# Kernel optimization log

Hardware: AMD Instinct MI355X
Metric: run time of the kernel (lower is better)

## Reference

```python
import jax, jax.numpy as jnp
import numpy as np

RAY_DIR = jnp.array([0.4395064455, 0.617598629942, 0.652231566745], dtype=jnp.float32)
TOL = 1e-7
CONTACT_THRESH = 25.0   # opt.contact_thresh
COLLISION_THRESH = 25.0  # opt.collision_thresh
BIG = 1e10


def mesh_contains(points, triangles, tri_valid):
    """Moller-Trumbore ray casting (fixed ray dir), parity test.
    points [B,P,3], triangles [B,T,3,3], tri_valid [B,T] -> exterior [B,P] bool."""
    v0, v1, v2 = triangles[:, :, 0, :], triangles[:, :, 1, :], triangles[:, :, 2, :]
    e1 = v1 - v0
    e2 = v2 - v0
    pvec = jnp.cross(jnp.broadcast_to(RAY_DIR, e2.shape), e2)          # [B,T,3]
    dets = jnp.sum(e1 * pvec, -1)                                      # [B,T]
    parallel = jnp.abs(dets) < TOL
    invdet = 1.0 / (dets + 0.1 * TOL)
    tvec = points[:, None, :, :] - v0[:, :, None, :]                   # [B,T,P,3]
    u = jnp.sum(tvec * pvec[:, :, None, :], -1) * invdet[:, :, None]   # [B,T,P]
    qvec = jnp.cross(tvec, e1[:, :, None, :])                          # [B,T,P,3]
    v = jnp.sum(qvec * RAY_DIR, -1) * invdet[:, :, None]
    t = jnp.sum(e2[:, :, None, :] * qvec, -1) * invdet[:, :, None]
    inter = (u > 0) & (u < 1) & (v > 0) & (u + v < 1) & (t > TOL)
    inter = inter & (~parallel & tri_valid)[:, :, None]
    n_hits = jnp.sum(inter.astype(jnp.int32), axis=1)                  # [B,P]
    return (n_hits % 2) == 0


def masked_mean_loss(vals, mask):
    m = mask.astype(vals.dtype)
    tot = m.sum()
    loss = jnp.where(tot > 0, (m * vals).sum() / jnp.maximum(tot, 1.0), 0.0)
    row = m.sum(1)
    losses = jnp.where(row > 0, (m * vals).sum(1) / jnp.maximum(row, 1.0), 0.0)
    return loss, losses


def setup_inputs() -> dict:
    key = jax.random.key(0)
    ks = jax.random.split(key, 6)
    B, Nh, Fh, No, Fo = 8, 778, 1538, 2000, 4000
    hand_verts = jax.random.normal(ks[0], (B, Nh, 3), dtype=jnp.float32)
    hand_faces = jax.random.randint(ks[1], (B, Fh, 3), 0, Nh, dtype=jnp.int32)
    obj_verts = jax.random.normal(ks[2], (B, No, 3), dtype=jnp.float32)
    obj_faces = jax.random.randint(ks[3], (B, Fo, 3), 0, 1200, dtype=jnp.int32)
    obj_vert_splits = 1200 + jax.random.randint(ks[4], (B,), 0, No - 1200 + 1, dtype=jnp.int32)
    obj_face_splits = 2400 + jax.random.randint(ks[5], (B,), 0, Fo - 2400 + 1, dtype=jnp.int32)
    return {"hand_verts": hand_verts, "hand_faces": hand_faces,
            "obj_verts": obj_verts, "obj_faces": obj_faces,
            "obj_vert_splits": obj_vert_splits, "obj_face_splits": obj_face_splits}


def reference(hand_verts, hand_faces, obj_verts, obj_faces, obj_vert_splits, obj_face_splits):
    B, Nh, _ = hand_verts.shape
    No = obj_verts.shape[1]
    Fo = obj_faces.shape[1]
    sg = jax.lax.stop_gradient

    # gather triangles (batched)
    hand_tri = jax.vmap(lambda v, f: v[f])(hand_verts, hand_faces)     # [B,Fh,3,3]
    obj_tri = jax.vmap(lambda v, f: v[f])(obj_verts, obj_faces)        # [B,Fo,3,3]

    face_valid = jnp.arange(Fo)[None, :] < obj_face_splits[:, None]    # [B,Fo]
    vert_valid = jnp.arange(No)[None, :] < obj_vert_splits[:, None]    # [B,No]

    # containment tests run on detached geometry (as in original)
    hand_tri_valid = jnp.ones(hand_tri.shape[:2], dtype=bool)
    exterior_obj = mesh_contains(sg(obj_verts), sg(hand_tri), hand_tri_valid)   # [B,No]
    exterior_hand = mesh_contains(sg(hand_verts), sg(obj_tri), face_valid)      # [B,Nh]

    penetr_o_mask = (~exterior_obj) & vert_valid
    penetr_h_mask = ~exterior_hand

    # ragged squared pairwise distances (bmm form of original), padded cols -> BIG
    rx = jnp.sum(hand_verts * hand_verts, -1)                          # [B,Nh]
    ry = jnp.sum(obj_verts * obj_verts, -1)                            # [B,No]
    zz = jnp.einsum('bnd,bmd->bnm', hand_verts, obj_verts)             # [B,Nh,No]
    dists = rx[:, :, None] + ry[:, None, :] - 2.0 * zz
    dists = jnp.where(vert_valid[:, None, :], dists, BIG)

    minoh_idxs = jnp.argmin(dists, axis=1)                             # [B,No]
    minho_idxs = jnp.argmin(dists, axis=2)                             # [B,Nh]

    results_close = jnp.take_along_axis(obj_verts, minho_idxs[:, :, None], axis=1)    # [B,Nh,3]
    results_o_close = jnp.take_along_axis(hand_verts, minoh_idxs[:, :, None], axis=1)  # [B,No,3]

    # contact_target == 'all'
    anchor_dists = jnp.sqrt(jnp.sum((results_close - hand_verts) ** 2, -1))    # [B,Nh]
    anchor_o_dist = jnp.sqrt(jnp.sum((results_o_close - obj_verts) ** 2, -1))  # [B,No]

    # contact_mode == 'dist_tanh' -> below_dist all ones
    contact_vals = CONTACT_THRESH * jnp.tanh(anchor_dists / CONTACT_THRESH)
    # collision_mode == 'dist_tanh'
    collision_vals = COLLISION_THRESH * jnp.tanh(anchor_dists / COLLISION_THRESH)
    collision_o_vals = COLLISION_THRESH * jnp.tanh(anchor_o_dist / COLLISION_THRESH)
    collision_o_vals = jnp.where(vert_valid, collision_o_vals, 0.0)

    # contact_zones == 'all'
    missed_mask = exterior_hand

    missed_loss, missed_losses = masked_mean_loss(contact_vals, missed_mask)
    penetr_h_loss, penetr_h_losses = masked_mean_loss(collision_vals, penetr_h_mask)
    penetr_o_loss, penetr_o_losses = masked_mean_loss(collision_o_vals, penetr_o_mask)
    penetr_loss = penetr_h_loss + penetr_o_loss
    penetr_losses = penetr_h_losses + penetr_o_losses

    return missed_loss, penetr_loss, missed_losses, penetr_losses
```

## Files before the change

### kernel.cpp

```cpp
#include <hip/hip_runtime.h>
#include <hip/hip_bf16.h>


#define RX 0.4395064455f
#define RY 0.617598629942f
#define RZ 0.652231566745f

#define MAXCHUNK_F4 512

struct Params {
    const float* hand_verts; const int* hand_faces;
    const float* obj_verts;  const int* obj_faces;
    const int* ovsplit; const int* ofsplit;
    int* hitsA;
    int* hitsB;
    float* anchor_h; float* anchor_o; float* partials;
    float* out;
    int B, Nh, Fh, No, Fo;
    int pbA, CA, chunkA, blocksA;
    int pbB, CB, chunkB, blocksB;
};

__device__ __forceinline__ void tri_pre_one(const float* __restrict__ vb,
                                            const int* __restrict__ f,
                                            float4* o) {
#pragma clang fp contract(off)
    int i0 = f[0], i1 = f[1], i2 = f[2];
    float v0x = vb[i0*3+0], v0y = vb[i0*3+1], v0z = vb[i0*3+2];
    float v1x = vb[i1*3+0], v1y = vb[i1*3+1], v1z = vb[i1*3+2];
    float v2x = vb[i2*3+0], v2y = vb[i2*3+1], v2z = vb[i2*3+2];
    float e1x = v1x - v0x, e1y = v1y - v0y, e1z = v1z - v0z;
    float e2x = v2x - v0x, e2y = v2y - v0y, e2z = v2z - v0z;
    float px = RY*e2z - RZ*e2y;
    float py = RZ*e2x - RX*e2z;
    float pz = RX*e2y - RY*e2x;
    float det = (e1x*px + e1y*py) + e1z*pz;
    float invdet = 1.0f / (det + 1e-8f);
    bool valid = !(fabsf(det) < 1e-7f);
    o[0] = make_float4(v0x, v0y, v0z, invdet);
    o[1] = make_float4(e1x, e1y, e1z, valid ? 1.0f : 0.0f);
    o[2] = make_float4(e2x, e2y, e2z, 0.0f);
    o[3] = make_float4(px,  py,  pz,  0.0f);
}

__device__ __forceinline__ void raycast_vb(const Params& p, int vbid, int tid,
                                           float4* s_tri) {
#pragma clang fp contract(off)
    const float* pts; const float* tverts; const int* tfaces; int* slots;
    int P, T, Nv, c, pb, b, chunk, tlim, plim;
    if (vbid < p.blocksA) {
        int per_b = p.pbA * p.CA;
        b  = vbid / per_b;
        int r = vbid - b * per_b;
        c  = r / p.pbA;
        pb = r - c * p.pbA;
        pts = p.obj_verts; tverts = p.hand_verts; tfaces = p.hand_faces;
        slots = p.hitsA;
        P = p.No; T = p.Fh; Nv = p.Nh; chunk = p.chunkA;
        tlim = p.Fh; plim = min(p.No, p.ovsplit[b]);
    } else {
        int j = vbid - p.blocksA;
        int per_b = p.pbB * p.CB;
        b  = j / per_b;
        int r = j - b * per_b;
        c  = r / p.pbB;
        pb = r - c * p.pbB;
        pts = p.hand_verts; tverts = p.obj_verts; tfaces = p.obj_faces;
        slots = p.hitsB;
        P = p.Nh; T = p.Fo; Nv = p.No; chunk = p.chunkB;
        tlim = min(p.Fo, p.ofsplit[b]); plim = p.Nh;
    }

    int tStart = c * chunk;
    if (tStart >= tlim) return;
    if (pb * 256 >= plim) return;
    int nTri = min(tStart + chunk, tlim) - tStart;

    if (tid < nTri) {
        int t = tStart + tid;
        tri_pre_one(tverts + (size_t)b * Nv * 3,
                    tfaces + ((size_t)b * T + t) * 3,
                    s_tri + (size_t)tid * 4);
    }

    int pp = pb * 256 + tid;
    bool act = pp < plim;
    float qx = 0.f, qy = 0.f, qz = 0.f;
    if (act) {
        const float* q = pts + ((size_t)b * P + pp) * 3;
        qx = q[0]; qy = q[1]; qz = q[2];
    }
    __syncthreads();

    if (act) {
        int cnt = 0;
        for (int i = 0; i < nTri; ++i) {
            const float4 f0 = s_tri[(i<<2)+0];
            const float4 f1 = s_tri[(i<<2)+1];
            const float4 f2 = s_tri[(i<<2)+2];
            const float4 f3 = s_tri[(i<<2)+3];
            float tvx = qx - f0.x, tvy = qy - f0.y, tvz = qz - f0.z;
            float u  = ((tvx*f3.x + tvy*f3.y) + tvz*f3.z) * f0.w;
            float qvx = tvy*f1.z - tvz*f1.y;
            float qvy = tvz*f1.x - tvx*f1.z;
            float qvz = tvx*f1.y - tvy*f1.x;
            float v  = ((qvx*RX + qvy*RY) + qvz*RZ) * f0.w;
            float tt = ((f2.x*qvx + f2.y*qvy) + f2.z*qvz) * f0.w;
            bool hit = (u > 0.0f) && (u < 1.0f) && (v > 0.0f) &&
                       ((u + v) < 1.0f) && (tt > 1e-7f) && (f1.w != 0.0f);
            cnt += hit ? 1 : 0;
        }
        slots[((size_t)(c * p.B + b)) * P + pp] = cnt;
    }
}

__device__ __forceinline__ void min_one(const Params& p, int w, int lane) {
#pragma clang fp contract(off)
    int nHand = p.B * p.Nh;
    const float* refv; const float* loopv; int loopN; float* outp;
    if (w < nHand) {
        int b = w / p.Nh;
        int n = w - b * p.Nh;
        refv  = p.hand_verts + ((size_t)b * p.Nh + n) * 3;
        loopv = p.obj_verts + (size_t)b * p.No * 3;
        loopN = p.ovsplit[b];
        outp  = p.anchor_h + (size_t)b * p.Nh + n;
    } else {
        int j = w - nHand;
        int b = j / p.No;
        int m = j - b * p.No;
        if (m >= p.ovsplit[b]) return;
        refv  = p.obj_verts + ((size_t)b * p.No + m) * 3;
        loopv = p.hand_verts + (size_t)b * p.Nh * 3;
        loopN = p.Nh;
        outp  = p.anchor_o + (size_t)b * p.No + m;
    }
    float hx = refv[0], hy = refv[1], hz = refv[2];
    float rx = (hx*hx + hy*hy) + hz*hz;
    unsigned long long best = ~0ull;
    for (int m = lane; m < loopN; m += 64) {
        float ox = loopv[m*3+0], oy = loopv[m*3+1], oz = loopv[m*3+2];
        float ry = (ox*ox + oy*oy) + oz*oz;
        float zz = (hx*ox + hy*oy) + hz*oz;
        float d = (rx + ry) - 2.0f * zz;
        unsigned long long e = ((unsigned long long)__float_as_uint(d) << 32) | (unsigned)m;
        if (e < best) best = e;
    }
    for (int off = 32; off > 0; off >>= 1) {
        unsigned long long o = __shfl_xor(best, off, 64);
        if (o < best) best = o;
    }
    if (lane == 0) {
        int idx = (best == ~0ull) ? 0 : (int)(best & 0xffffffffu);
        const float* cv = loopv + (size_t)idx * 3;
        float dx = cv[0] - hx, dy = cv[1] - hy, dz = cv[2] - hz;
        *outp = sqrtf((dx*dx + dy*dy) + dz*dz);
    }
}

__global__ __launch_bounds__(256) void mega(Params p) {
    __shared__ float4 s_tri[MAXCHUNK_F4];
    const int tid = threadIdx.x;
    const int bid = blockIdx.x;
    const int nRay = p.blocksA + p.blocksB;
    if (bid < nRay) {
        raycast_vb(p, bid, tid, s_tri);
    } else {
        int w = (bid - nRay) * 4 + (tid >> 6);
        if (w < p.B * (p.Nh + p.No)) min_one(p, w, tid & 63);
    }
}

__global__ __launch_bounds__(1024) void reduce8(Params p) {
    const int b = blockIdx.x, tid = threadIdx.x;
    const int wave = tid >> 6, lane = tid & 63;
    float s0=0.f,s1=0.f,s2=0.f,s3=0.f,s4=0.f,s5=0.f;

    int tlimB = min(p.Fo, p.ofsplit[b]);
    int nCB = (tlimB + p.chunkB - 1) / p.chunkB;
    for (int n = tid; n < p.Nh; n += 1024) {
        int par = 0;
        for (int c = 0; c < nCB; ++c)
            par += p.hitsB[((size_t)(c * p.B + b)) * p.Nh + n];
        bool ext = (par & 1) == 0;
        float val = 25.0f * tanhf(p.anchor_h[(size_t)b*p.Nh + n] / 25.0f);
        if (ext) { s0 += val; s1 += 1.0f; } else { s2 += val; s3 += 1.0f; }
    }
    int split = p.ovsplit[b];
    for (int m = tid; m < split; m += 1024) {
        int par = 0;
        for (int c = 0; c < p.CA; ++c)
            par += p.hitsA[((size_t)(c * p.B + b)) * p.No + m];
        if (par & 1) {
            s4 += 25.0f * tanhf(p.anchor_o[(size_t)b*p.No + m] / 25.0f);
            s5 += 1.0f;
        }
    }
    for (int off = 32; off > 0; off >>= 1) {
        s0 += __shfl_xor(s0, off, 64);
        s1 += __shfl_xor(s1, off, 64);
        s2 += __shfl_xor(s2, off, 64);
        s3 += __shfl_xor(s3, off, 64);
        s4 += __shfl_xor(s4, off, 64);
        s5 += __shfl_xor(s5, off, 64);
    }
    __shared__ float red[16][6];
    if (lane == 0) {
        red[wave][0]=s0; red[wave][1]=s1; red[wave][2]=s2;
        red[wave][3]=s3; red[wave][4]=s4; red[wave][5]=s5;
    }
    __syncthreads();
    if (tid == 0) {
        float t0=0.f,t1=0.f,t2=0.f,t3=0.f,t4=0.f,t5=0.f;
        for (int wv = 0; wv < 16; ++wv) {
            t0 += red[wv][0]; t1 += red[wv][1]; t2 += red[wv][2];
            t3 += red[wv][3]; t4 += red[wv][4]; t5 += red[wv][5];
        }
        p.out[2 + b]  = (t1 > 0.f) ? t0 / fmaxf(t1, 1.f) : 0.f;
        float ph      = (t3 > 0.f) ? t2 / fmaxf(t3, 1.f) : 0.f;
        float po      = (t5 > 0.f) ? t4 / fmaxf(t5, 1.f) : 0.f;
        p.out[10 + b] = ph + po;
        float* pp = p.partials + b * 6;
        pp[0]=t0; pp[1]=t1; pp[2]=t2; pp[3]=t3; pp[4]=t4; pp[5]=t5;
    }
}

__global__ void fin(Params p) {
    if (threadIdx.x == 0 && blockIdx.x == 0) {
        float sm=0.f,cm=0.f,sph=0.f,cph=0.f,spo=0.f,cpo=0.f;
        for (int b = 0; b < p.B; ++b) {
            const float* pp = p.partials + b * 6;
            sm  += pp[0]; cm  += pp[1]; sph += pp[2];
            cph += pp[3]; spo += pp[4]; cpo += pp[5];
        }
        float missed = (cm  > 0.f) ? sm  / fmaxf(cm , 1.f) : 0.f;
        float ph     = (cph > 0.f) ? sph / fmaxf(cph, 1.f) : 0.f;
        float po     = (cpo > 0.f) ? spo / fmaxf(cpo, 1.f) : 0.f;
        p.out[0] = missed;
        p.out[1] = ph + po;
    }
}

extern "C" void kernel_launch(void* const* d_in, const int* in_sizes, int n_in,
                              void* d_out, int out_size, void* d_ws, size_t ws_size,
                              hipStream_t stream) {
    Params p;
    p.hand_verts = (const float*)d_in[0];
    p.hand_faces = (const int*)d_in[1];
    p.obj_verts  = (const float*)d_in[2];
    p.obj_faces  = (const int*)d_in[3];
    p.ovsplit    = (const int*)d_in[4];
    p.ofsplit    = (const int*)d_in[5];
    p.out        = (float*)d_out;

    p.B  = in_sizes[4];
    p.Nh = in_sizes[0] / (3 * p.B);
    p.Fh = in_sizes[1] / (3 * p.B);
    p.No = in_sizes[2] / (3 * p.B);
    p.Fo = in_sizes[3] / (3 * p.B);

    p.CA = 16; p.CB = 32;
    p.chunkA = (p.Fh + p.CA - 1) / p.CA;
    p.chunkB = (p.Fo + p.CB - 1) / p.CB;
    p.pbA = (p.No + 255) / 256;
    p.pbB = (p.Nh + 255) / 256;
    p.blocksA = p.pbA * p.CA * p.B;
    p.blocksB = p.pbB * p.CB * p.B;

    char* ws = (char*)d_ws;
    size_t off = 0;
    auto alloc = [&](size_t bytes) -> void* {
        void* q = ws + off;
        off = (off + bytes + 255) & ~(size_t)255;
        return q;
    };
    p.hitsA    = (int*)   alloc((size_t)p.CA * p.B * p.No * sizeof(int));
    p.hitsB    = (int*)   alloc((size_t)p.CB * p.B * p.Nh * sizeof(int));
    p.anchor_h = (float*) alloc((size_t)p.B * p.Nh * sizeof(float));
    p.anchor_o = (float*) alloc((size_t)p.B * p.No * sizeof(float));
    p.partials = (float*) alloc((size_t)p.B * 6 * sizeof(float));

    int totalMin  = p.B * (p.Nh + p.No);
    int nMinBlocks = (totalMin + 3) / 4;
    int grid = p.blocksA + p.blocksB + nMinBlocks;

    mega<<<grid, 256, 0, stream>>>(p);
    reduce8<<<p.B, 1024, 0, stream>>>(p);
    fin<<<1, 64, 0, stream>>>(p);
}
```

Measured before the change: 147.9 us.

## Process two points per thread in raycast and fuse final reduction via last-block atomic

Each raycast thread now tests two query points against every triangle in shared memory, so each LDS read of a triangle is reused twice and half as many blocks are launched. The separate finalization kernel is folded into the per-batch reduction kernel using a done counter and last-block detection, removing one launch. The cost is fewer blocks for a GPU with many CUs, which may reduce parallelism and latency hiding. The counter is reset inside mega before reduce_fin runs.

After: 134.6 us (median of 2 runs). 9.0% less time.

```diff
diff --git a/kernel.cpp b/kernel.cpp
--- a/kernel.cpp
+++ b/kernel.cpp
@@ -7,6 +7,7 @@
 #define RZ 0.652231566745f
 
 #define MAXCHUNK_F4 512
+#define PTS_PER_BLK 512
 
 struct Params {
     const float* hand_verts; const int* hand_faces;
@@ -15,6 +16,7 @@
     int* hitsA;
     int* hitsB;
     float* anchor_h; float* anchor_o; float* partials;
+    unsigned int* done;
     float* out;
     int B, Nh, Fh, No, Fo;
     int pbA, CA, chunkA, blocksA;
@@ -41,6 +43,22 @@
     o[1] = make_float4(e1x, e1y, e1z, valid ? 1.0f : 0.0f);
     o[2] = make_float4(e2x, e2y, e2z, 0.0f);
     o[3] = make_float4(px,  py,  pz,  0.0f);
+}
+
+__device__ __forceinline__ int mt_test(float qx, float qy, float qz,
+                                       const float4& f0, const float4& f1,
+                                       const float4& f2, const float4& f3) {
+#pragma clang fp contract(off)
+    float tvx = qx - f0.x, tvy = qy - f0.y, tvz = qz - f0.z;
+    float u  = ((tvx*f3.x + tvy*f3.y) + tvz*f3.z) * f0.w;
+    float qvx = tvy*f1.z - tvz*f1.y;
+    float qvy = tvz*f1.x - tvx*f1.z;
+    float qvz = tvx*f1.y - tvy*f1.x;
+    float v  = ((qvx*RX + qvy*RY) + qvz*RZ) * f0.w;
+    float tt = ((f2.x*qvx + f2.y*qvy) + f2.z*qvz) * f0.w;
+    bool hit = (u > 0.0f) && (u < 1.0f) && (v > 0.0f) &&
+               ((u + v) < 1.0f) && (tt > 1e-7f) && (f1.w != 0.0f);
+    return hit ? 1 : 0;
 }
 
 __device__ __forceinline__ void raycast_vb(const Params& p, int vbid, int tid,
@@ -73,7 +91,7 @@
 
     int tStart = c * chunk;
     if (tStart >= tlim) return;
-    if (pb * 256 >= plim) return;
+    if (pb * PTS_PER_BLK >= plim) return;
     int nTri = min(tStart + chunk, tlim) - tStart;
 
     if (tid < nTri) {
@@ -83,35 +101,34 @@
                     s_tri + (size_t)tid * 4);
     }
 
-    int pp = pb * 256 + tid;
-    bool act = pp < plim;
-    float qx = 0.f, qy = 0.f, qz = 0.f;
-    if (act) {
-        const float* q = pts + ((size_t)b * P + pp) * 3;
-        qx = q[0]; qy = q[1]; qz = q[2];
+    int p1 = pb * PTS_PER_BLK + tid;
+    int p2 = p1 + 256;
+    bool act1 = p1 < plim, act2 = p2 < plim;
+    float q1x = 0.f, q1y = 0.f, q1z = 0.f;
+    float q2x = 0.f, q2y = 0.f, q2z = 0.f;
+    if (act1) {
+        const float* q = pts + ((size_t)b * P + p1) * 3;
+        q1x = q[0]; q1y = q[1]; q1z = q[2];
+    }
+    if (act2) {
+        const float* q = pts + ((size_t)b * P + p2) * 3;
+        q2x = q[0]; q2y = q[1]; q2z = q[2];
     }
     __syncthreads();
 
-    if (act) {
-        int cnt = 0;
-        for (int i = 0; i < nTri; ++i) {
-            const float4 f0 = s_tri[(i<<2)+0];
-            const float4 f1 = s_tri[(i<<2)+1];
-            const float4 f2 = s_tri[(i<<2)+2];
-            const float4 f3 = s_tri[(i<<2)+3];
-            float tvx = qx - f0.x, tvy = qy - f0.y, tvz = qz - f0.z;
-            float u  = ((tvx*f3.x + tvy*f3.y) + tvz*f3.z) * f0.w;
-            float qvx = tvy*f1.z - tvz*f1.y;
-            float qvy = tvz*f1.x - tvx*f1.z;
-            float qvz = tvx*f1.y - tvy*f1.x;
-            float v  = ((qvx*RX + qvy*RY) + qvz*RZ) * f0.w;
-            float tt = ((f2.x*qvx + f2.y*qvy) + f2.z*qvz) * f0.w;
-            bool hit = (u > 0.0f) && (u < 1.0f) && (v > 0.0f) &&
-                       ((u + v) < 1.0f) && (tt > 1e-7f) && (f1.w != 0.0f);
-            cnt += hit ? 1 : 0;
-        }
-        slots[((size_t)(c * p.B + b)) * P + pp] = cnt;
-    }
+    if (!act1) return;
+    int cnt1 = 0, cnt2 = 0;
+    for (int i = 0; i < nTri; ++i) {
+        const float4 f0 = s_tri[(i<<2)+0];
+        const float4 f1 = s_tri[(i<<2)+1];
+        const float4 f2 = s_tri[(i<<2)+2];
+        const float4 f3 = s_tri[(i<<2)+3];
+        cnt1 += mt_test(q1x, q1y, q1z, f0, f1, f2, f3);
+        cnt2 += mt_test(q2x, q2y, q2z, f0, f1, f2, f3);
+    }
+    int* base = slots + ((size_t)(c * p.B + b)) * P;
+    base[p1] = cnt1;
+    if (act2) base[p2] = cnt2;
 }
 
 __device__ __forceinline__ void min_one(const Params& p, int w, int lane) {
@@ -162,6 +179,7 @@
     __shared__ float4 s_tri[MAXCHUNK_F4];
     const int tid = threadIdx.x;
     const int bid = blockIdx.x;
+    if (bid == 0 && tid == 0) *p.done = 0u;
     const int nRay = p.blocksA + p.blocksB;
     if (bid < nRay) {
         raycast_vb(p, bid, tid, s_tri);
@@ -171,7 +189,7 @@
     }
 }
 
-__global__ __launch_bounds__(1024) void reduce8(Params p) {
+__global__ __launch_bounds__(1024) void reduce_fin(Params p) {
     const int b = blockIdx.x, tid = threadIdx.x;
     const int wave = tid >> 6, lane = tid & 63;
     float s0=0.f,s1=0.f,s2=0.f,s3=0.f,s4=0.f,s5=0.f;
@@ -205,6 +223,7 @@
         s5 += __shfl_xor(s5, off, 64);
     }
     __shared__ float red[16][6];
+    __shared__ bool s_last;
     if (lane == 0) {
         red[wave][0]=s0; red[wave][1]=s1; red[wave][2]=s2;
         red[wave][3]=s3; red[wave][4]=s4; red[wave][5]=s5;
@@ -222,23 +241,24 @@
         p.out[10 + b] = ph + po;
         float* pp = p.partials + b * 6;
         pp[0]=t0; pp[1]=t1; pp[2]=t2; pp[3]=t3; pp[4]=t4; pp[5]=t5;
-    }
-}
-
-__global__ void fin(Params p) {
-    if (threadIdx.x == 0 && blockIdx.x == 0) {
-        float sm=0.f,cm=0.f,sph=0.f,cph=0.f,spo=0.f,cpo=0.f;
-        for (int b = 0; b < p.B; ++b) {
-            const float* pp = p.partials + b * 6;
-            sm  += pp[0]; cm  += pp[1]; sph += pp[2];
-            cph += pp[3]; spo += pp[4]; cpo += pp[5];
-        }
-        float missed = (cm  > 0.f) ? sm  / fmaxf(cm , 1.f) : 0.f;
-        float ph     = (cph > 0.f) ? sph / fmaxf(cph, 1.f) : 0.f;
-        float po     = (cpo > 0.f) ? spo / fmaxf(cpo, 1.f) : 0.f;
-        p.out[0] = missed;
-        p.out[1] = ph + po;
-    }
+        __threadfence();
+        unsigned int old = atomicAdd(p.done, 1u);
+        s_last = (old == (unsigned int)(gridDim.x - 1));
+    }
+    __syncthreads();
+    if (!s_last || tid != 0) return;
+    __threadfence();
+    float sm=0.f,cm=0.f,sph=0.f,cph=0.f,spo=0.f,cpo=0.f;
+    for (int bb = 0; bb < p.B; ++bb) {
+        const float* pp = p.partials + bb * 6;
+        sm  += pp[0]; cm  += pp[1]; sph += pp[2];
+        cph += pp[3]; spo += pp[4]; cpo += pp[5];
+    }
+    float missed = (cm  > 0.f) ? sm  / fmaxf(cm , 1.f) : 0.f;
+    float ph     = (cph > 0.f) ? sph / fmaxf(cph, 1.f) : 0.f;
+    float po     = (cpo > 0.f) ? spo / fmaxf(cpo, 1.f) : 0.f;
+    p.out[0] = missed;
+    p.out[1] = ph + po;
 }
 
 extern "C" void kernel_launch(void* const* d_in, const int* in_sizes, int n_in,
@@ -262,8 +282,8 @@
     p.CA = 16; p.CB = 32;
     p.chunkA = (p.Fh + p.CA - 1) / p.CA;
     p.chunkB = (p.Fo + p.CB - 1) / p.CB;
-    p.pbA = (p.No + 255) / 256;
-    p.pbB = (p.Nh + 255) / 256;
+    p.pbA = (p.No + PTS_PER_BLK - 1) / PTS_PER_BLK;
+    p.pbB = (p.Nh + PTS_PER_BLK - 1) / PTS_PER_BLK;
     p.blocksA = p.pbA * p.CA * p.B;
     p.blocksB = p.pbB * p.CB * p.B;
 
@@ -279,12 +299,12 @@
     p.anchor_h = (float*) alloc((size_t)p.B * p.Nh * sizeof(float));
     p.anchor_o = (float*) alloc((size_t)p.B * p.No * sizeof(float));
     p.partials = (float*) alloc((size_t)p.B * 6 * sizeof(float));
-
-    int totalMin  = p.B * (p.Nh + p.No);
+    p.done     = (unsigned int*)alloc(sizeof(unsigned int));
+
+    int totalMin   = p.B * (p.Nh + p.No);
     int nMinBlocks = (totalMin + 3) / 4;
     int grid = p.blocksA + p.blocksB + nMinBlocks;
 
     mega<<<grid, 256, 0, stream>>>(p);
-    reduce8<<<p.B, 1024, 0, stream>>>(p);
-    fin<<<1, 64, 0, stream>>>(p);
-}
+    reduce_fin<<<p.B, 1024, 0, stream>>>(p);
+}
```
